# Kernel tuning notes

Measured on AMD Instinct MI355X. Metric: run time of the kernel, lower is better.

## Reference

```python
import jax, jax.numpy as jnp
import numpy as np

HEAD_NUM = 16
HEAD_SIZE = 64
D_MODEL = 1024
B, N = 8, 1024
MASK_PENALTY = 1e8


def setup_inputs() -> dict:
    key = jax.random.key(0)
    k1, k2, k3 = jax.random.split(key, 3)
    inputs = jax.random.normal(k1, (B, N, D_MODEL), dtype=jnp.float32)
    mask = jax.random.randint(k2, (B, N), 0, 2).astype(jnp.float32)
    # glorot-uniform-ish init for kernel [H, 3, d_model, head_size]
    limit = float(np.sqrt(6.0 / (D_MODEL + HEAD_SIZE)))
    kernel = jax.random.uniform(k3, (HEAD_NUM, 3, D_MODEL, HEAD_SIZE),
                                dtype=jnp.float32, minval=-limit, maxval=limit)
    return {"inputs": inputs, "mask": mask, "kernel": kernel}


def reference(inputs, mask, kernel):
    # inputs: [B,N,d], kernel: [H,3,d,s]
    q = jnp.einsum('bnd,hds->bhns', inputs, kernel[:, 0])
    k = jnp.einsum('bnd,hds->bhns', inputs, kernel[:, 1])
    v = jnp.einsum('bnd,hds->bhns', inputs, kernel[:, 2])
    # NOTE: original never applies 1/sqrt(head_size) scaling (faithful).
    scores = jnp.einsum('bhns,bhms->bhnm', q, k)  # [B,H,N,N]
    # additive mask: outer product of padding mask, penalty on masked pairs
    pair_mask = mask[:, None, :, None] * mask[:, None, None, :]  # [B,1,N,N]
    scores = scores - MASK_PENALTY * (1.0 - pair_mask)
    attn = jax.nn.softmax(scores, axis=-1)
    out = jnp.einsum('bhnm,bhms->bhns', attn, v)  # [B,H,N,s]
    # original permutes to [B,N,s,H] then flattens -> head axis fastest
    out = jnp.transpose(out, (0, 2, 3, 1))  # [B,N,s,H]
    return out.reshape(out.shape[0], out.shape[1], HEAD_SIZE * HEAD_NUM)
```

## Files before the change

### kernel.cpp

```cpp
#include <hip/hip_runtime.h>
#include <math.h>

#define BB 8
#define NN 1024
#define DD 1024
#define HH 16
#define SS 64
#define BH (BB*HH)

typedef _Float16 half8 __attribute__((ext_vector_type(8)));
typedef _Float16 half4v __attribute__((ext_vector_type(4)));
typedef float floatx4 __attribute__((ext_vector_type(4)));

#define MFMA16(A, B, C) __builtin_amdgcn_mfma_f32_16x16x32_f16((A), (B), (C), 0, 0, 0)

__device__ __forceinline__ void gload16(const _Float16* g, _Float16* l) {
    __builtin_amdgcn_global_load_lds(
        (const __attribute__((address_space(1))) void*)g,
        (__attribute__((address_space(3))) void*)l,
        16, 0, 0);
}

__global__ __launch_bounds__(256) void split_x(
    const float* __restrict__ X, _Float16* __restrict__ Xh, _Float16* __restrict__ Xl)
{
    int idx = (blockIdx.x * 256 + threadIdx.x) * 4;
    float4 x4 = *(const float4*)(X + idx);
    float xs[4] = {x4.x, x4.y, x4.z, x4.w};
    half4v h, l;
    #pragma unroll
    for (int i = 0; i < 4; i++) {
        _Float16 hi = (_Float16)xs[i];
        h[i] = hi;
        l[i] = (_Float16)(xs[i] - (float)hi);
    }
    *(half4v*)(Xh + idx) = h;
    *(half4v*)(Xl + idx) = l;
}

__global__ __launch_bounds__(256) void split_wt(
    const float* __restrict__ W, _Float16* __restrict__ Wth, _Float16* __restrict__ Wtl)
{
    __shared__ float tile[64][68];
    const int hc = blockIdx.x, d0 = blockIdx.y * 64;
    const int t = threadIdx.x;
    {
        int i = t >> 2, sq = (t & 3) * 16;
        const float* src = W + ((size_t)hc * DD + d0 + i) * SS + sq;
        #pragma unroll
        for (int u = 0; u < 4; u++) {
            float4 v = *(const float4*)(src + 4 * u);
            tile[i][sq + 4 * u + 0] = v.x; tile[i][sq + 4 * u + 1] = v.y;
            tile[i][sq + 4 * u + 2] = v.z; tile[i][sq + 4 * u + 3] = v.w;
        }
    }
    __syncthreads();
    {
        int s = t >> 2, jq = (t & 3) * 16;
        _Float16 hbuf[16], lbuf[16];
        #pragma unroll
        for (int u = 0; u < 16; u++) {
            float x = tile[jq + u][s];
            _Float16 hi = (_Float16)x;
            hbuf[u] = hi;
            lbuf[u] = (_Float16)(x - (float)hi);
        }
        size_t off = (size_t)hc * SS * DD + (size_t)s * DD + d0 + jq;
        *(half8*)(Wth + off)     = *(half8*)(hbuf);
        *(half8*)(Wth + off + 8) = *(half8*)(hbuf + 8);
        *(half8*)(Wtl + off)     = *(half8*)(lbuf);
        *(half8*)(Wtl + off + 8) = *(half8*)(lbuf + 8);
    }
}

__global__ __launch_bounds__(256, 2) void qkv_mfma(
    const _Float16* __restrict__ Xh, const _Float16* __restrict__ Xl,
    const _Float16* __restrict__ Wth, const _Float16* __restrict__ Wtl,
    _Float16* __restrict__ Qh, _Float16* __restrict__ Ql,
    _Float16* __restrict__ Kh, _Float16* __restrict__ Kl,
    _Float16* __restrict__ Vt)
{
    const int flat = blockIdx.y * 64 + blockIdx.x;
    const int swz  = (flat & 7) * 192 + (flat >> 3);
    const int bx = swz & 63;
    const int by = swz >> 6;
    const int hc0 = by * 2;
    const int r0  = bx * 128;

    const int tid = threadIdx.x;
    const int wave = tid >> 6, lane = tid & 63;
    const int l16 = lane & 15, quad = lane >> 4;
    const int wr = wave >> 1, wc = wave & 1;

    __shared__ _Float16 sAh[128 * 32];
    __shared__ _Float16 sAl[128 * 32];
    __shared__ _Float16 sBh[128 * 32];
    __shared__ _Float16 sBl[128 * 32];

    floatx4 acc[4][4];
    #pragma unroll
    for (int i = 0; i < 4; i++)
        #pragma unroll
        for (int j = 0; j < 4; j++) acc[i][j] = (floatx4){0.f, 0.f, 0.f, 0.f};

    const _Float16* Ab_h = Xh  + (size_t)r0 * DD;
    const _Float16* Ab_l = Xl  + (size_t)r0 * DD;
    const _Float16* Bb_h = Wth + (size_t)hc0 * SS * DD;
    const _Float16* Bb_l = Wtl + (size_t)hc0 * SS * DD;

    for (int k0 = 0; k0 < DD; k0 += 32) {
        #pragma unroll
        for (int i = 0; i < 2; i++) {
            const int g = tid + 256 * i;
            const int row = g >> 2, kc = (g & 3) * 8;
            const size_t go = (size_t)row * DD + k0 + kc;
            gload16(Ab_h + go, &sAh[g * 8]);
            gload16(Ab_l + go, &sAl[g * 8]);
            gload16(Bb_h + go, &sBh[g * 8]);
            gload16(Bb_l + go, &sBl[g * 8]);
        }
        __syncthreads();

        half8 Ah[4], Al[4], Bh[4], Bl[4];
        #pragma unroll
        for (int t = 0; t < 4; t++) {
            const int ar = wr * 64 + 16 * t + l16;
            const int br = wc * 64 + 16 * t + l16;
            Ah[t] = *(const half8*)&sAh[ar * 32 + quad * 8];
            Al[t] = *(const half8*)&sAl[ar * 32 + quad * 8];
            Bh[t] = *(const half8*)&sBh[br * 32 + quad * 8];
            Bl[t] = *(const half8*)&sBl[br * 32 + quad * 8];
        }
        #pragma unroll
        for (int i = 0; i < 4; i++)
            #pragma unroll
            for (int j = 0; j < 4; j++)
                acc[i][j] = MFMA16(Ah[i], Bh[j], acc[i][j]);
        #pragma unroll
        for (int i = 0; i < 4; i++)
            #pragma unroll
            for (int j = 0; j < 4; j++)
                acc[i][j] = MFMA16(Ah[i], Bl[j], acc[i][j]);
        #pragma unroll
        for (int i = 0; i < 4; i++)
            #pragma unroll
            for (int j = 0; j < 4; j++)
                acc[i][j] = MFMA16(Al[i], Bh[j], acc[i][j]);
        __syncthreads();
    }

    const int hc = hc0 + wc;
    const int h = hc / 3, c = hc % 3;
    const int rowbase = r0 + wr * 64;
    if (c == 2) {
        #pragma unroll
        for (int i = 0; i < 4; i++)
            #pragma unroll
            for (int j = 0; j < 4; j++) {
                int tok0 = rowbase + 16 * i + 4 * quad;
                int b = tok0 >> 10, n0 = tok0 & 1023;
                half4v pk;
                #pragma unroll
                for (int r = 0; r < 4; r++) pk[r] = (_Float16)acc[i][j][r];
                *(half4v*)(Vt + ((size_t)(b * HH + h) * SS + 16 * j + l16) * NN + n0) = pk;
            }
    } else {
        _Float16* Ph = (c == 0) ? Qh : Kh;
        _Float16* Pl = (c == 0) ? Ql : Kl;
        #pragma unroll
        for (int i = 0; i < 4; i++)
            #pragma unroll
            for (int j = 0; j < 4; j++)
                #pragma unroll
                for (int r = 0; r < 4; r++) {
                    int tok = rowbase + 16 * i + 4 * quad + r;
                    int b = tok >> 10, n = tok & 1023;
                    float v = acc[i][j][r];
                    _Float16 vh = (_Float16)v;
                    _Float16 vl = (_Float16)(v - (float)vh);
                    size_t off = ((size_t)(b * HH + h) * NN + n) * SS + 16 * j + l16;
                    Ph[off] = vh; Pl[off] = vl;
                }
    }
}

__global__ __launch_bounds__(256) void attn_mfma(
    const _Float16* __restrict__ Qh, const _Float16* __restrict__ Ql,
    const _Float16* __restrict__ Kh, const _Float16* __restrict__ Kl,
    const _Float16* __restrict__ Vt,
    const float* __restrict__ mask,
    float* __restrict__ out)
{
    const int bh = blockIdx.x, qt = blockIdx.y;
    const int b = bh >> 4, h = bh & 15;
    const int tid = threadIdx.x;
    const int wave = tid >> 6, lane = tid & 63;
    const int l16 = lane & 15, quad = lane >> 4;

    __shared__ float Ms[NN];
    __shared__ _Float16 KhS[64 * 64];
    __shared__ _Float16 KlS[64 * 64];
    __shared__ _Float16 VS [64 * 64];
    __shared__ _Float16 Plds[4][32][72];

    *(float4*)&Ms[tid * 4] = *(const float4*)(mask + b * NN + tid * 4);

    half8 G[6];
    auto stage_load = [&](int kt_) {
        #pragma unroll
        for (int i = 0; i < 2; i++) {
            int g = tid + 256 * i;
            int row = g >> 3;
            int c = (g & 7) ^ (row & 7);
            size_t ko = ((size_t)bh * NN + kt_ * 64 + row) * SS + c * 8;
            G[i]     = *(const half8*)(Kh + ko);
            G[2 + i] = *(const half8*)(Kl + ko);
            G[4 + i] = *(const half8*)(Vt + ((size_t)bh * SS + row) * NN
                                       + (size_t)kt_ * 64 + c * 8);
        }
    };
    auto stage_store = [&]() {
        #pragma unroll
        for (int i = 0; i < 2; i++) {
            int g = tid + 256 * i;
            *(half8*)&KhS[g * 8] = G[i];
            *(half8*)&KlS[g * 8] = G[2 + i];
            *(half8*)&VS [g * 8] = G[4 + i];
        }
    };

    stage_load(0);
    stage_store();
    __syncthreads();

    const int qrow0 = qt * 128 + wave * 32;
    half8 Aqh[2][2], Aql[2][2];
    #pragma unroll
    for (int g = 0; g < 2; g++) {
        const size_t qbase = ((size_t)bh * NN + qrow0 + 16 * g + l16) * SS + quad * 8;
        Aqh[g][0] = *(const half8*)(Qh + qbase);
        Aqh[g][1] = *(const half8*)(Qh + qbase + 32);
        Aql[g][0] = *(const half8*)(Ql + qbase);
        Aql[g][1] = *(const half8*)(Ql + qbase + 32);
    }

    float qm[2][4], m_old[2][4], l_sum[2][4];
    floatx4 accO[2][4];
    #pragma unroll
    for (int g = 0; g < 2; g++) {
        #pragma unroll
        for (int r = 0; r < 4; r++) {
            qm[g][r] = Ms[qrow0 + 16 * g + quad * 4 + r];
            m_old[g][r] = -3.0e38f;
            l_sum[g][r] = 0.f;
        }
        #pragma unroll
        for (int j = 0; j < 4; j++) accO[g][j] = (floatx4){0.f, 0.f, 0.f, 0.f};
    }

    const int sw = l16 & 7;

    for (int kt = 0; kt < 16; kt++) {
        if (kt < 15) stage_load(kt + 1);

        floatx4 accS[2][4];
        #pragma unroll
        for (int g = 0; g < 2; g++)
            #pragma unroll
            for (int jt = 0; jt < 4; jt++) accS[g][jt] = (floatx4){0.f, 0.f, 0.f, 0.f};
        #pragma unroll
        for (int jt = 0; jt < 4; jt++) {
            const int rowK = jt * 16 + l16;
            const _Float16* krh = &KhS[rowK * 64];
            const _Float16* krl = &KlS[rowK * 64];
            half8 Bh0 = *(const half8*)&krh[((quad    ) ^ sw) * 8];
            half8 Bh1 = *(const half8*)&krh[((quad + 4) ^ sw) * 8];
            half8 Bl0 = *(const half8*)&krl[((quad    ) ^ sw) * 8];
            half8 Bl1 = *(const half8*)&krl[((quad + 4) ^ sw) * 8];
            #pragma unroll
            for (int g = 0; g < 2; g++) {
                accS[g][jt] = MFMA16(Aqh[g][0], Bh0, accS[g][jt]);
                accS[g][jt] = MFMA16(Aqh[g][1], Bh1, accS[g][jt]);
                accS[g][jt] = MFMA16(Aqh[g][0], Bl0, accS[g][jt]);
                accS[g][jt] = MFMA16(Aqh[g][1], Bl1, accS[g][jt]);
                accS[g][jt] = MFMA16(Aql[g][0], Bh0, accS[g][jt]);
                accS[g][jt] = MFMA16(Aql[g][1], Bh1, accS[g][jt]);
            }
        }
        float km[4];
        #pragma unroll
        for (int jt = 0; jt < 4; jt++) km[jt] = Ms[kt * 64 + jt * 16 + l16];
        #pragma unroll
        for (int g = 0; g < 2; g++)
            #pragma unroll
            for (int jt = 0; jt < 4; jt++)
                #pragma unroll
                for (int r = 0; r < 4; r++)
                    accS[g][jt][r] -= 1.0e8f * (1.0f - qm[g][r] * km[jt]);

        #pragma unroll
        for (int g = 0; g < 2; g++) {
            float alpha[4];
            #pragma unroll
            for (int r = 0; r < 4; r++) {
                float mt = fmaxf(fmaxf(accS[g][0][r], accS[g][1][r]),
                                 fmaxf(accS[g][2][r], accS[g][3][r]));
                #pragma unroll
                for (int off = 1; off < 16; off <<= 1)
                    mt = fmaxf(mt, __shfl_xor(mt, off, 64));
                float mn = fmaxf(m_old[g][r], mt);
                alpha[r] = __expf(m_old[g][r] - mn);
                m_old[g][r] = mn;
                float ls = 0.f;
                #pragma unroll
                for (int jt = 0; jt < 4; jt++) {
                    float pj = __expf(accS[g][jt][r] - mn);
                    accS[g][jt][r] = pj;
                    ls += pj;
                }
                #pragma unroll
                for (int off = 1; off < 16; off <<= 1)
                    ls += __shfl_xor(ls, off, 64);
                l_sum[g][r] = l_sum[g][r] * alpha[r] + ls;
            }
            #pragma unroll
            for (int j = 0; j < 4; j++)
                #pragma unroll
                for (int r = 0; r < 4; r++)
                    accO[g][j][r] *= alpha[r];

            #pragma unroll
            for (int jt = 0; jt < 4; jt++)
                #pragma unroll
                for (int r = 0; r < 4; r++)
                    Plds[wave][16 * g + quad * 4 + r][((jt ^ quad) << 4) + l16] =
                        (_Float16)accS[g][jt][r];
        }

        #pragma unroll
        for (int ks = 0; ks < 2; ks++) {
            int cbase = (((2 * ks + (quad >> 1)) ^ (l16 >> 2)) << 4) + (quad & 1) * 8;
            half8 Ap[2];
            #pragma unroll
            for (int g = 0; g < 2; g++)
                Ap[g] = *(const half8*)&Plds[wave][16 * g + l16][cbase];
            #pragma unroll
            for (int j = 0; j < 4; j++) {
                half8 Bv = *(const half8*)&VS[(j * 16 + l16) * 64
                                              + (((ks * 4 + quad) ^ sw) * 8)];
                #pragma unroll
                for (int g = 0; g < 2; g++)
                    accO[g][j] = MFMA16(Ap[g], Bv, accO[g][j]);
            }
        }

        if (kt < 15) {
            __syncthreads();
            stage_store();
            __syncthreads();
        }
    }

    #pragma unroll
    for (int g = 0; g < 2; g++)
        #pragma unroll
        for (int r = 0; r < 4; r++) {
            float inv = 1.f / l_sum[g][r];
            int qrow = qrow0 + 16 * g + quad * 4 + r;
            #pragma unroll
            for (int j = 0; j < 4; j++)
                out[((size_t)(b * NN + qrow)) * (SS * HH) + (j * 16 + l16) * HH + h] =
                    accO[g][j][r] * inv;
        }
}

__global__ __launch_bounds__(256) void qkv_kernel(
    const float* __restrict__ X, const float* __restrict__ W, float* __restrict__ qkv)
{
    const int ttile = blockIdx.x;
    const int hc    = blockIdx.y;
    const int h     = hc / 3, c = hc % 3;
    const int tid = threadIdx.x;
    const int tx = tid & 15, ty = tid >> 4;
    __shared__ float As[32][68];
    __shared__ float Bs[32][68];
    const float* Wb = W + (size_t)hc * DD * SS;
    const int row0 = ttile * 64;
    float acc[4][4];
    #pragma unroll
    for (int i = 0; i < 4; i++)
        #pragma unroll
        for (int j = 0; j < 4; j++) acc[i][j] = 0.f;
    for (int k0 = 0; k0 < DD; k0 += 32) {
        #pragma unroll
        for (int l = 0; l < 2; l++) {
            int i = tid + l * 256;
            int r = i >> 3;
            int kq = (i & 7) * 4;
            float4 x4 = *(const float4*)(X + (size_t)(row0 + r) * DD + k0 + kq);
            As[kq + 0][r] = x4.x; As[kq + 1][r] = x4.y;
            As[kq + 2][r] = x4.z; As[kq + 3][r] = x4.w;
        }
        #pragma unroll
        for (int l = 0; l < 2; l++) {
            int i = tid + l * 256;
            int kr = i >> 4;
            int sq = (i & 15) * 4;
            *(float4*)&Bs[kr][sq] = *(const float4*)(Wb + (size_t)(k0 + kr) * SS + sq);
        }
        __syncthreads();
        #pragma unroll
        for (int kk = 0; kk < 32; kk++) {
            float4 a4 = *(const float4*)&As[kk][ty * 4];
            float4 b4 = *(const float4*)&Bs[kk][tx * 4];
            float a[4] = {a4.x, a4.y, a4.z, a4.w};
            float bb[4] = {b4.x, b4.y, b4.z, b4.w};
            #pragma unroll
            for (int i = 0; i < 4; i++)
                #pragma unroll
                for (int j = 0; j < 4; j++)
                    acc[i][j] = fmaf(a[i], bb[j], acc[i][j]);
        }
        __syncthreads();
    }
    float* outp = qkv + (size_t)c * BH * NN * SS;
    #pragma unroll
    for (int i = 0; i < 4; i++) {
        int tg = row0 + ty * 4 + i;
        int b = tg >> 10, n = tg & 1023;
        float4 v4 = make_float4(acc[i][0], acc[i][1], acc[i][2], acc[i][3]);
        *(float4*)(outp + ((size_t)(b * HH + h) * NN + n) * SS + tx * 4) = v4;
    }
}

__global__ __launch_bounds__(256) void attn_kernel(
    const float* __restrict__ qkv,
    const float* __restrict__ mask,
    float* __restrict__ out)
{
    const int qt = blockIdx.x, h = blockIdx.y, b = blockIdx.z;
    const int tid = threadIdx.x;
    const int tx = tid & 15, ty = tid >> 4;
    const int bh = b * HH + h;
    const float* Q = qkv + (size_t)bh * NN * SS;
    const float* K = qkv + (size_t)BH * NN * SS + (size_t)bh * NN * SS;
    const float* V = qkv + 2 * (size_t)BH * NN * SS + (size_t)bh * NN * SS;

    __shared__ float QsT[64][68];
    __shared__ float KsT[64][68];
    __shared__ float Vs [64][68];
    __shared__ float PsT[64][68];
    __shared__ float Ms[NN];

    {
        float4 mm = *(const float4*)(mask + b * NN + tid * 4);
        *(float4*)&Ms[tid * 4] = mm;
    }
    #pragma unroll
    for (int l = 0; l < 4; l++) {
        int i = tid + l * 256;
        int r = i >> 4, sq = (i & 15) * 4;
        float4 x4 = *(const float4*)(Q + (size_t)(qt * 64 + r) * SS + sq);
        QsT[sq + 0][r] = x4.x; QsT[sq + 1][r] = x4.y;
        QsT[sq + 2][r] = x4.z; QsT[sq + 3][r] = x4.w;
    }
    __syncthreads();

    float m_old[4], l_sum[4], O[4][4], qm[4];
    #pragma unroll
    for (int i = 0; i < 4; i++) {
        qm[i] = Ms[qt * 64 + ty * 4 + i];
        m_old[i] = -3.0e38f; l_sum[i] = 0.f;
        #pragma unroll
        for (int j = 0; j < 4; j++) O[i][j] = 0.f;
    }

    for (int kt = 0; kt < 16; kt++) {
        #pragma unroll
        for (int l = 0; l < 4; l++) {
            int i = tid + l * 256;
            int r = i >> 4, sq = (i & 15) * 4;
            float4 k4 = *(const float4*)(K + (size_t)(kt * 64 + r) * SS + sq);
            KsT[sq + 0][r] = k4.x; KsT[sq + 1][r] = k4.y;
            KsT[sq + 2][r] = k4.z; KsT[sq + 3][r] = k4.w;
            float4 v4 = *(const float4*)(V + (size_t)(kt * 64 + r) * SS + sq);
            *(float4*)&Vs[r][sq] = v4;
        }
        __syncthreads();

        float sc[4][4];
        #pragma unroll
        for (int i = 0; i < 4; i++)
            #pragma unroll
            for (int j = 0; j < 4; j++) sc[i][j] = 0.f;
        #pragma unroll 8
        for (int s = 0; s < 64; s++) {
            float4 a4 = *(const float4*)&QsT[s][ty * 4];
            float4 b4 = *(const float4*)&KsT[s][tx * 4];
            float a[4] = {a4.x, a4.y, a4.z, a4.w};
            float bb[4] = {b4.x, b4.y, b4.z, b4.w};
            #pragma unroll
            for (int i = 0; i < 4; i++)
                #pragma unroll
                for (int j = 0; j < 4; j++)
                    sc[i][j] = fmaf(a[i], bb[j], sc[i][j]);
        }
        float km[4];
        #pragma unroll
        for (int j = 0; j < 4; j++) km[j] = Ms[kt * 64 + tx * 4 + j];
        #pragma unroll
        for (int i = 0; i < 4; i++)
            #pragma unroll
            for (int j = 0; j < 4; j++) {
                float pen = 1.0e8f * (1.0f - qm[i] * km[j]);
                sc[i][j] = sc[i][j] - pen;
            }

        #pragma unroll
        for (int i = 0; i < 4; i++) {
            float mt = fmaxf(fmaxf(sc[i][0], sc[i][1]), fmaxf(sc[i][2], sc[i][3]));
            #pragma unroll
            for (int off = 1; off < 16; off <<= 1)
                mt = fmaxf(mt, __shfl_xor(mt, off, 64));
            float mn = fmaxf(m_old[i], mt);
            float alpha = __expf(m_old[i] - mn);
            float p[4];
            #pragma unroll
            for (int j = 0; j < 4; j++) p[j] = __expf(sc[i][j] - mn);
            float ls = (p[0] + p[1]) + (p[2] + p[3]);
            #pragma unroll
            for (int off = 1; off < 16; off <<= 1)
                ls += __shfl_xor(ls, off, 64);
            l_sum[i] = l_sum[i] * alpha + ls;
            m_old[i] = mn;
            #pragma unroll
            for (int j = 0; j < 4; j++) {
                O[i][j] *= alpha;
                PsT[tx * 4 + j][ty * 4 + i] = p[j];
            }
        }
        __syncthreads();

        #pragma unroll 8
        for (int kj = 0; kj < 64; kj++) {
            float4 p4 = *(const float4*)&PsT[kj][ty * 4];
            float4 v4 = *(const float4*)&Vs[kj][tx * 4];
            float p[4] = {p4.x, p4.y, p4.z, p4.w};
            float vv[4] = {v4.x, v4.y, v4.z, v4.w};
            #pragma unroll
            for (int i = 0; i < 4; i++)
                #pragma unroll
                for (int j = 0; j < 4; j++)
                    O[i][j] = fmaf(p[i], vv[j], O[i][j]);
        }
        __syncthreads();
    }

    #pragma unroll
    for (int i = 0; i < 4; i++) {
        int qrow = qt * 64 + ty * 4 + i;
        float inv = 1.f / l_sum[i];
        #pragma unroll
        for (int j = 0; j < 4; j++) {
            int s = tx * 4 + j;
            out[((size_t)(b * NN + qrow)) * (SS * HH) + s * HH + h] = O[i][j] * inv;
        }
    }
}

extern "C" void kernel_launch(void* const* d_in, const int* in_sizes, int n_in,
                              void* d_out, int out_size, void* d_ws, size_t ws_size,
                              hipStream_t stream) {
    const float* X    = (const float*)d_in[0];
    const float* mask = (const float*)d_in[1];
    const float* W    = (const float*)d_in[2];
    float* out = (float*)d_out;

    const size_t x_elems  = (size_t)BB * NN * DD;
    const size_t w_elems  = (size_t)HH * 3 * SS * DD;
    const size_t qk_elems = (size_t)BH * NN * SS;
    const size_t need_fast = (2 * x_elems + 2 * w_elems + 5 * qk_elems) * sizeof(_Float16);

    if (ws_size >= need_fast) {
        _Float16* Xh  = (_Float16*)d_ws;
        _Float16* Xl  = Xh  + x_elems;
        _Float16* Wth = Xl  + x_elems;
        _Float16* Wtl = Wth + w_elems;
        _Float16* Qh  = Wtl + w_elems;
        _Float16* Ql  = Qh  + qk_elems;
        _Float16* Kh  = Ql  + qk_elems;
        _Float16* Kl  = Kh  + qk_elems;
        _Float16* Vt  = Kl  + qk_elems;

        split_x<<<dim3((unsigned)(x_elems / 1024)), dim3(256), 0, stream>>>(X, Xh, Xl);
        split_wt<<<dim3(48, 16), dim3(256), 0, stream>>>(W, Wth, Wtl);
        qkv_mfma<<<dim3(64, 24), dim3(256), 0, stream>>>(Xh, Xl, Wth, Wtl, Qh, Ql, Kh, Kl, Vt);
        attn_mfma<<<dim3(128, 8), dim3(256), 0, stream>>>(Qh, Ql, Kh, Kl, Vt, mask, out);
    } else if (ws_size >= 3ull * BH * NN * SS * sizeof(float)) {
        float* qkv = (float*)d_ws;
        qkv_kernel<<<dim3(128, 48), dim3(256), 0, stream>>>(X, W, qkv);
        attn_kernel<<<dim3(16, 16, 8), dim3(256), 0, stream>>>(qkv, mask, out);
    }
}
```

Baseline: 461.7 us.

## Transpose QK^T MFMA so each lane owns a query row in softmax

Swaps the MFMA operands for S = QK^T so the accumulator holds S transposed. Each lane then owns one query row and four key columns per tile. The row max and row sum mostly reduce in-register, with two cross-lane shuffles instead of eight shuffle steps per row. P is also written to LDS as packed half4 without the XOR swizzle. The rescale factors and final normalizers must be broadcast back to the output layout with extra shuffles, and the unswizzled P layout may add LDS bank conflicts.

```diff
diff --git a/kernel.cpp b/kernel.cpp
--- a/kernel.cpp
+++ b/kernel.cpp
@@ -244,16 +244,13 @@
         Aql[g][1] = *(const half8*)(Ql + qbase + 32);
     }
 
-    float qm[2][4], m_old[2][4], l_sum[2][4];
+    float qm[2], m_old[2], l_sum[2];
     floatx4 accO[2][4];
     #pragma unroll
     for (int g = 0; g < 2; g++) {
-        #pragma unroll
-        for (int r = 0; r < 4; r++) {
-            qm[g][r] = Ms[qrow0 + 16 * g + quad * 4 + r];
-            m_old[g][r] = -3.0e38f;
-            l_sum[g][r] = 0.f;
-        }
+        qm[g] = Ms[qrow0 + 16 * g + l16];
+        m_old[g] = -3.0e38f;
+        l_sum[g] = 0.f;
         #pragma unroll
         for (int j = 0; j < 4; j++) accO[g][j] = (floatx4){0.f, 0.f, 0.f, 0.f};
     }
@@ -279,71 +276,87 @@
             half8 Bl1 = *(const half8*)&krl[((quad + 4) ^ sw) * 8];
             #pragma unroll
             for (int g = 0; g < 2; g++) {
-                accS[g][jt] = MFMA16(Aqh[g][0], Bh0, accS[g][jt]);
-                accS[g][jt] = MFMA16(Aqh[g][1], Bh1, accS[g][jt]);
-                accS[g][jt] = MFMA16(Aqh[g][0], Bl0, accS[g][jt]);
-                accS[g][jt] = MFMA16(Aqh[g][1], Bl1, accS[g][jt]);
-                accS[g][jt] = MFMA16(Aql[g][0], Bh0, accS[g][jt]);
-                accS[g][jt] = MFMA16(Aql[g][1], Bh1, accS[g][jt]);
+                accS[g][jt] = MFMA16(Bh0, Aqh[g][0], accS[g][jt]);
+                accS[g][jt] = MFMA16(Bh1, Aqh[g][1], accS[g][jt]);
+                accS[g][jt] = MFMA16(Bl0, Aqh[g][0], accS[g][jt]);
+                accS[g][jt] = MFMA16(Bl1, Aqh[g][1], accS[g][jt]);
+                accS[g][jt] = MFMA16(Bh0, Aql[g][0], accS[g][jt]);
+                accS[g][jt] = MFMA16(Bh1, Aql[g][1], accS[g][jt]);
             }
         }
-        float km[4];
-        #pragma unroll
-        for (int jt = 0; jt < 4; jt++) km[jt] = Ms[kt * 64 + jt * 16 + l16];
+
+        float km[4][4];
+        #pragma unroll
+        for (int jt = 0; jt < 4; jt++) {
+            float4 k4 = *(const float4*)&Ms[kt * 64 + jt * 16 + quad * 4];
+            km[jt][0] = k4.x; km[jt][1] = k4.y; km[jt][2] = k4.z; km[jt][3] = k4.w;
+        }
         #pragma unroll
         for (int g = 0; g < 2; g++)
             #pragma unroll
             for (int jt = 0; jt < 4; jt++)
                 #pragma unroll
                 for (int r = 0; r < 4; r++)
-                    accS[g][jt][r] -= 1.0e8f * (1.0f - qm[g][r] * km[jt]);
+                    accS[g][jt][r] -= 1.0e8f * (1.0f - qm[g] * km[jt][r]);
 
         #pragma unroll
         for (int g = 0; g < 2; g++) {
-            float alpha[4];
-            #pragma unroll
-            for (int r = 0; r < 4; r++) {
-                float mt = fmaxf(fmaxf(accS[g][0][r], accS[g][1][r]),
-                                 fmaxf(accS[g][2][r], accS[g][3][r]));
-                #pragma unroll
-                for (int off = 1; off < 16; off <<= 1)
-                    mt = fmaxf(mt, __shfl_xor(mt, off, 64));
-                float mn = fmaxf(m_old[g][r], mt);
-                alpha[r] = __expf(m_old[g][r] - mn);
-                m_old[g][r] = mn;
-                float ls = 0.f;
-                #pragma unroll
-                for (int jt = 0; jt < 4; jt++) {
-                    float pj = __expf(accS[g][jt][r] - mn);
-                    accS[g][jt][r] = pj;
-                    ls += pj;
-                }
-                #pragma unroll
-                for (int off = 1; off < 16; off <<= 1)
-                    ls += __shfl_xor(ls, off, 64);
-                l_sum[g][r] = l_sum[g][r] * alpha[r] + ls;
+            float a0 = fmaxf(fmaxf(accS[g][0][0], accS[g][0][1]),
+                             fmaxf(accS[g][0][2], accS[g][0][3]));
+            float a1 = fmaxf(fmaxf(accS[g][1][0], accS[g][1][1]),
+                             fmaxf(accS[g][1][2], accS[g][1][3]));
+            float a2 = fmaxf(fmaxf(accS[g][2][0], accS[g][2][1]),
+                             fmaxf(accS[g][2][2], accS[g][2][3]));
+            float a3 = fmaxf(fmaxf(accS[g][3][0], accS[g][3][1]),
+                             fmaxf(accS[g][3][2], accS[g][3][3]));
+            float mt = fmaxf(fmaxf(a0, a1), fmaxf(a2, a3));
+            mt = fmaxf(mt, __shfl_xor(mt, 16, 64));
+            mt = fmaxf(mt, __shfl_xor(mt, 32, 64));
+            float mn = fmaxf(m_old[g], mt);
+            float alpha = __expf(m_old[g] - mn);
+            m_old[g] = mn;
+
+            float sj[4];
+            #pragma unroll
+            for (int jt = 0; jt < 4; jt++) {
+                float p0 = __expf(accS[g][jt][0] - mn);
+                float p1 = __expf(accS[g][jt][1] - mn);
+                float p2 = __expf(accS[g][jt][2] - mn);
+                float p3 = __expf(accS[g][jt][3] - mn);
+                accS[g][jt][0] = p0; accS[g][jt][1] = p1;
+                accS[g][jt][2] = p2; accS[g][jt][3] = p3;
+                sj[jt] = (p0 + p1) + (p2 + p3);
             }
+            float ls = (sj[0] + sj[1]) + (sj[2] + sj[3]);
+            ls += __shfl_xor(ls, 16, 64);
+            ls += __shfl_xor(ls, 32, 64);
+            l_sum[g] = l_sum[g] * alpha + ls;
+
+            float alphaO[4];
+            #pragma unroll
+            for (int r = 0; r < 4; r++)
+                alphaO[r] = __shfl(alpha, quad * 4 + r, 64);
             #pragma unroll
             for (int j = 0; j < 4; j++)
                 #pragma unroll
                 for (int r = 0; r < 4; r++)
-                    accO[g][j][r] *= alpha[r];
-
-            #pragma unroll
-            for (int jt = 0; jt < 4; jt++)
-                #pragma unroll
-                for (int r = 0; r < 4; r++)
-                    Plds[wave][16 * g + quad * 4 + r][((jt ^ quad) << 4) + l16] =
-                        (_Float16)accS[g][jt][r];
+                    accO[g][j][r] *= alphaO[r];
+
+            #pragma unroll
+            for (int jt = 0; jt < 4; jt++) {
+                half4v pk;
+                #pragma unroll
+                for (int r = 0; r < 4; r++) pk[r] = (_Float16)accS[g][jt][r];
+                *(half4v*)&Plds[wave][16 * g + l16][jt * 16 + quad * 4] = pk;
+            }
         }
 
         #pragma unroll
         for (int ks = 0; ks < 2; ks++) {
-            int cbase = (((2 * ks + (quad >> 1)) ^ (l16 >> 2)) << 4) + (quad & 1) * 8;
             half8 Ap[2];
             #pragma unroll
             for (int g = 0; g < 2; g++)
-                Ap[g] = *(const half8*)&Plds[wave][16 * g + l16][cbase];
+                Ap[g] = *(const half8*)&Plds[wave][16 * g + l16][ks * 32 + quad * 8];
             #pragma unroll
             for (int j = 0; j < 4; j++) {
                 half8 Bv = *(const half8*)&VS[(j * 16 + l16) * 64
@@ -362,16 +375,20 @@
     }
 
     #pragma unroll
-    for (int g = 0; g < 2; g++)
+    for (int g = 0; g < 2; g++) {
+        float inv[4];
+        #pragma unroll
+        for (int r = 0; r < 4; r++)
+            inv[r] = 1.f / __shfl(l_sum[g], quad * 4 + r, 64);
         #pragma unroll
         for (int r = 0; r < 4; r++) {
-            float inv = 1.f / l_sum[g][r];
             int qrow = qrow0 + 16 * g + quad * 4 + r;
             #pragma unroll
             for (int j = 0; j < 4; j++)
                 out[((size_t)(b * NN + qrow)) * (SS * HH) + (j * 16 + l16) * HH + h] =
-                    accO[g][j][r] * inv;
-        }
+                    accO[g][j][r] * inv[r];
+        }
+    }
 }
 
 __global__ __launch_bounds__(256) void qkv_kernel(
```

After: 421.6 us. 8.7% less time.
